# Kernel optimization log

Measured on AMD Instinct MI355X. Metric: run time of the kernel, lower is better.

## Reference

```python
import jax, jax.numpy as jnp
import numpy as np

T, B, H, IN = 2048, 4096, 51, 2

def setup_inputs() -> dict:
    key = jax.random.key(0)
    ks = jax.random.split(key, 12)
    s = 1.0 / np.sqrt(H)
    u = lambda k, shape: jax.random.uniform(k, shape, jnp.float32, -s, s)
    return {
        "input": jax.random.normal(ks[0], (T, B, IN), jnp.float32),
        "W_ih1": u(ks[1], (4 * H, IN)),
        "W_hh1": u(ks[2], (4 * H, H)),
        "b_ih1": u(ks[3], (4 * H,)),
        "b_hh1": u(ks[4], (4 * H,)),
        "W_ih2": u(ks[5], (4 * H, H)),
        "W_hh2": u(ks[6], (4 * H, H)),
        "b_ih2": u(ks[7], (4 * H,)),
        "b_hh2": u(ks[8], (4 * H,)),
        "W_lin": u(ks[9], (1, H)),
        "b_lin": u(ks[10], (1,)),
    }

def _lstm_cell(x, h, c, W_ih, W_hh, b_ih, b_hh):
    # PyTorch LSTMCell gate order: input, forget, cell(g), output
    gates = x @ W_ih.T + b_ih + h @ W_hh.T + b_hh  # [B, 4H]
    i, f, g, o = jnp.split(gates, 4, axis=-1)
    c_new = jax.nn.sigmoid(f) * c + jax.nn.sigmoid(i) * jnp.tanh(g)
    h_new = jax.nn.sigmoid(o) * jnp.tanh(c_new)
    return h_new, c_new

def reference(input, W_ih1, W_hh1, b_ih1, b_hh1, W_ih2, W_hh2, b_ih2, b_hh2, W_lin, b_lin):
    Bsz = input.shape[1]
    z = jnp.zeros((Bsz, H), input.dtype)

    def step(carry, x_t):
        h1, c1, h2, c2 = carry
        h1, c1 = _lstm_cell(x_t, h1, c1, W_ih1, W_hh1, b_ih1, b_hh1)
        h2, c2 = _lstm_cell(h1, h2, c2, W_ih2, W_hh2, b_ih2, b_hh2)
        out = h2 @ W_lin.T + b_lin  # [B, 1]
        return (h1, c1, h2, c2), out[:, 0]

    _, outs = jax.lax.scan(step, (z, z, z, z), input)  # outs: [T, B]
    return outs.T  # [B, T] == torch.stack(outputs, 1).squeeze(2)
```

## Files before the change

kernel.cpp:

```cpp
#include <hip/hip_runtime.h>

namespace {
constexpr int T    = 2048;
constexpr int Bsz  = 4096;
constexpr int H    = 51;
constexpr int H4   = 204;
constexpr int NB   = 16;
constexpr int BLK  = 1024;
constexpr int GRID = Bsz / NB;
constexpr int NITER = T + 4;
constexpr float SCI  = -1.44269504f;
constexpr float SCGP =  2.88539008f;
constexpr float SC2  = -2.88539008f;
}

typedef float    f32x4 __attribute__((ext_vector_type(4)));
typedef _Float16 f16x8 __attribute__((ext_vector_type(8)));
typedef unsigned short u16;

__device__ __forceinline__ float RCP(float x)  { return __builtin_amdgcn_rcpf(x); }
__device__ __forceinline__ float EXP2(float x) { return __builtin_amdgcn_exp2f(x); }

__device__ __forceinline__ float lstm_act(float Gi, float Gf, float Gg, float Go, float& c) {
  float ei = EXP2(Gi), ef = EXP2(Gf), eo = EXP2(Go), eg = EXP2(Gg);
  float pi = 1.f + ei, pf = 1.f + ef, pg = 1.f + eg, po = 1.f + eo;
  float pig = pi * pg;
  float num = fmaf(c, pig, (eg - 1.f) * pf);
  c = num * RCP(pig * pf);
  float ec = EXP2(SC2 * fabsf(c));
  float tc = copysignf(1.f - ec, c);
  return tc * RCP((1.f + ec) * po);
}

#define BAR() asm volatile("s_waitcnt lgkmcnt(0)\n\ts_barrier" ::: "memory")
#define MF(A, B, C) __builtin_amdgcn_mfma_f32_16x16x32_f16((A), (B), (C), 0, 0, 0)


__global__ __launch_bounds__(BLK, 4) void lstm2_v10(
    const float* __restrict__ x,
    const float* __restrict__ Wih1, const float* __restrict__ Whh1,
    const float* __restrict__ bih1, const float* __restrict__ bhh1,
    const float* __restrict__ Wih2, const float* __restrict__ Whh2,
    const float* __restrict__ bih2, const float* __restrict__ bhh2,
    const float* __restrict__ Wlin, const float* __restrict__ blin,
    float* __restrict__ out) {
  extern __shared__ __align__(16) char smraw[];
  u16*   PL1 = (u16*)smraw;
  u16*   PL2 = (u16*)(smraw + 8192);
  auto   XB  = (float2 (*)[32][16])(smraw + 12288);
  auto   OB  = (float (*)[16][40])(smraw + 20480);
  float* SW  = (float*)smraw;

  const int tid  = threadIdx.x;
  const int lane = tid & 63;
  const int wid  = tid >> 6;
  const int a    = lane & 15;
  const int q    = lane >> 4;
  const int b0   = blockIdx.x * NB;
  const int rb   = lane * 8;

  bool isL1 = false; int tA = -1, tB = -1;
  switch (wid) {
    case 0:  isL1 = true; tA = 0;  tB = 1;  break;
    case 1:  isL1 = true; tA = 4;  tB = 5;  break;
    case 2:  isL1 = true; tA = 8;  tB = 9;  break;
    case 3:  isL1 = true; tA = 10; tB = 11; break;
    case 4:  isL1 = true; tA = 2;  tB = 3;  break;
    case 5:  isL1 = true; tA = 6;  tB = 7;  break;
    case 6:  tA = 6;  tB = 7;  break;
    case 7:  isL1 = true; tA = 12; break;
    case 8:  tA = 0;  tB = 1;  break;
    case 9:  tA = 3;  tB = 4;  break;
    case 10: tA = 8;  tB = 9;  break;
    case 11: tA = 10; tB = 11; break;
    case 12: tA = 2;  break;
    case 13: tA = 5;  break;
    case 14: break;
    case 15: tA = 12; break;
  }
  const bool isHead = (wid == 14);
  const bool isXinj = (wid == 15);
  const bool isL2   = (!isL1) && (tA >= 0);

  f16x8 wA[2][4];
  f16x8 hA[2];

  for (int i = tid; i < H4 * H; i += BLK) SW[i] = Whh1[i];
  __syncthreads();
  if (isL1) {
#pragma unroll
    for (int ti = 0; ti < 2; ++ti) {
      const int t = ti ? tB : tA;
      if (t >= 0) {
        const int  rp   = 16 * t + a;
        const bool vld  = (rp < H4);
        const int  gate = rp & 3;
        const int  wrow = gate * H + (rp >> 2);
        const float sc  = (gate == 2) ? SCGP : SCI;
#pragma unroll
        for (int sp = 0; sp < 2; ++sp)
#pragma unroll
          for (int j = 0; j < 8; ++j) {
            const int k = 32 * sp + 16 * (j >> 2) + 4 * q + (j & 3);
            float val = 0.f;
            if (vld) {
              if (k < H)           val = SW[wrow * H + k];
              else if (k == H)     val = Wih1[wrow * 2 + 0];
              else if (k == H + 1) val = Wih1[wrow * 2 + 1];
              else if (k == H + 2) val = bih1[wrow] + bhh1[wrow];
            }
            wA[ti][sp][j] = (_Float16)(val * sc);
          }
      }
    }
  }
  __syncthreads();
  for (int i = tid; i < H4 * H; i += BLK) SW[i] = Wih2[i];
  __syncthreads();
  if (isL2) {
#pragma unroll
    for (int ti = 0; ti < 2; ++ti) {
      const int t = ti ? tB : tA;
      if (t >= 0) {
        const int  rp   = 16 * t + a;
        const bool vld  = (rp < H4);
        const int  gate = rp & 3;
        const int  wrow = gate * H + (rp >> 2);
        const float sc  = (gate == 2) ? SCGP : SCI;
#pragma unroll
        for (int sp = 0; sp < 2; ++sp)
#pragma unroll
          for (int j = 0; j < 8; ++j) {
            const int k = 32 * sp + 16 * (j >> 2) + 4 * q + (j & 3);
            float val = 0.f;
            if (vld) {
              if (k < H)           val = SW[wrow * H + k];
              else if (k == H + 2) val = bih2[wrow] + bhh2[wrow];
            }
            wA[ti][sp][j] = (_Float16)(val * sc);
          }
      }
    }
  }
  __syncthreads();
  for (int i = tid; i < H4 * H; i += BLK) SW[i] = Whh2[i];
  __syncthreads();
  if (isL2) {
#pragma unroll
    for (int ti = 0; ti < 2; ++ti) {
      const int t = ti ? tB : tA;
      if (t >= 0) {
        const int  rp   = 16 * t + a;
        const bool vld  = (rp < H4);
        const int  gate = rp & 3;
        const int  wrow = gate * H + (rp >> 2);
        const float sc  = (gate == 2) ? SCGP : SCI;
#pragma unroll
        for (int sp = 2; sp < 4; ++sp)
#pragma unroll
          for (int j = 0; j < 8; ++j) {
            const int kp = 32 * (sp - 2) + 16 * (j >> 2) + 4 * q + (j & 3);
            float val = (vld && kp < H) ? SW[wrow * H + kp] * sc : 0.f;
            wA[ti][sp][j] = (_Float16)val;
          }
      }
    }
  }
  if (isHead) {
#pragma unroll
    for (int sp = 0; sp < 2; ++sp)
#pragma unroll
      for (int j = 0; j < 8; ++j) {
        const int kp = 32 * sp + 16 * (j >> 2) + 4 * q + (j & 3);
        float val = 0.f;
        if (a == 0) {
          if (kp < H)           val = Wlin[kp];
          else if (kp == H + 2) val = blin[0];
        }
        hA[sp][j] = (_Float16)val;
      }
  }
  __syncthreads();

  for (int i = tid; i < 6144; i += BLK) PL1[i] = 0;
  if (isXinj) {
#pragma unroll
    for (int k = 0; k < 4; ++k) {
      const int idx = lane + 64 * k, st = idx >> 3, bc = (idx & 7) * 2;
      *(float4*)&XB[0][st][bc] = *(const float4*)(x + ((size_t)st * Bsz + b0 + bc) * 2);
    }
  }
  __syncthreads();
  if (tid < 16) {
#pragma unroll
    for (int buf = 0; buf < 4; ++buf) PL1[buf * 1024 + 512 + (tid + 16) * 8 + 5] = 0x3C00;
#pragma unroll
    for (int buf = 0; buf < 2; ++buf) PL2[buf * 1024 + 512 + (tid + 16) * 8 + 5] = 0x3C00;
  }
  __syncthreads();
  const int xslot = ((lane >> 4) == 0) ? (lane & 15) * 8 + 7 : ((lane & 15) + 16) * 8 + 4;
  if (isXinj && lane < 32) {
    const float xv = ((const float*)&XB[0][0][0])[(lane & 15) * 2 + (lane >> 4)];
    *(_Float16*)&PL1[3 * 1024 + 512 + xslot] = (_Float16)xv;
  }
  __syncthreads();

  int  widx0 = 0, widx1 = 0;
  bool uval0 = false, uval1 = false;
  if (tA >= 0) {
    const int u = 4 * tA + q;
    if (u < H) {
      uval0 = true;
      const int spl = u >> 5, kl = u & 31;
      widx0 = spl * 512 + (a + 16 * ((kl >> 2) & 3)) * 8 + ((kl & 3) + 4 * (kl >> 4));
    }
  }
  if (tB >= 0) {
    const int u = 4 * tB + q;
    if (u < H) {
      uval1 = true;
      const int spl = u >> 5, kl = u & 31;
      widx1 = spl * 512 + (a + 16 * ((kl >> 2) & 3)) * 8 + ((kl & 3) + 4 * (kl >> 4));
    }
  }

  float cc0 = 0.f, cc1 = 0.f;
  const f32x4 z4 = {0.f, 0.f, 0.f, 0.f};

  if (isL1) {
    f16x8 pf0 = *(const f16x8*)&PL1[3 * 1024 + rb];
    f16x8 pf1 = *(const f16x8*)&PL1[3 * 1024 + 512 + rb];

#define L1B(S, B)                                                               \
  { const int s = (S);                                                          \
    f32x4 dA = MF(wA[0][0], pf0, z4); dA = MF(wA[0][1], pf1, dA);               \
    f32x4 dB = z4;                                                              \
    if (tB >= 0) { dB = MF(wA[1][0], pf0, z4); dB = MF(wA[1][1], pf1, dB); }    \
    if (s < T) {                                                                \
      const float h0 = lstm_act(dA[0], dA[1], dA[2], dA[3], cc0);               \
      if (uval0) *(_Float16*)&PL1[(B) * 1024 + widx0] = (_Float16)h0;           \
      if (tB >= 0) {                                                            \
        const float h1 = lstm_act(dB[0], dB[1], dB[2], dB[3], cc1);             \
        if (uval1) *(_Float16*)&PL1[(B) * 1024 + widx1] = (_Float16)h1;         \
      }                                                                         \
    }                                                                           \
    BAR();                                                                      \
    pf0 = *(const f16x8*)&PL1[(B) * 1024 + rb];                                 \
    pf1 = *(const f16x8*)&PL1[(B) * 1024 + 512 + rb];                           \
  }

    for (int s0 = 0; s0 < NITER; s0 += 4) {
      L1B(s0 + 0, 0) L1B(s0 + 1, 1) L1B(s0 + 2, 2) L1B(s0 + 3, 3)
    }
#undef L1B
  } else {
    f16x8 pc0 = *(const f16x8*)&PL1[2 * 1024 + rb];
    f16x8 pc1 = *(const f16x8*)&PL1[2 * 1024 + 512 + rb];
    float4 xcr0 = {0,0,0,0}, xcr1 = {0,0,0,0}, xcr2 = {0,0,0,0}, xcr3 = {0,0,0,0};

#define BB(S, B)                                                                \
  { const int s = (S); constexpr int P = (B) & 1;                               \
    f16x8 bq0 = *(const f16x8*)&PL2[(P ^ 1) * 1024 + rb];                       \
    f16x8 bq1 = *(const f16x8*)&PL2[(P ^ 1) * 1024 + 512 + rb];                 \
    if (isXinj) {                                                               \
      const int ph = s & 31;                                                    \
      if (ph == 0) {                                                            \
        if (s + 32 < T) {                                                       \
          const int i0 = lane, i1 = lane + 64, i2 = lane + 128, i3 = lane + 192;\
          xcr0 = *(const float4*)(x + ((size_t)(s + 32 + (i0 >> 3)) * Bsz + b0 + (i0 & 7) * 2) * 2); \
          xcr1 = *(const float4*)(x + ((size_t)(s + 32 + (i1 >> 3)) * Bsz + b0 + (i1 & 7) * 2) * 2); \
          xcr2 = *(const float4*)(x + ((size_t)(s + 32 + (i2 >> 3)) * Bsz + b0 + (i2 & 7) * 2) * 2); \
          xcr3 = *(const float4*)(x + ((size_t)(s + 32 + (i3 >> 3)) * Bsz + b0 + (i3 & 7) * 2) * 2); \
        }                                                                       \
      } else if (ph == 1) {                                                     \
        if (s + 31 < T) {                                                       \
          const int buf = ((s >> 5) + 1) & 1;                                   \
          const int i0 = lane, i1 = lane + 64, i2 = lane + 128, i3 = lane + 192;\
          *(float4*)&XB[buf][i0 >> 3][(i0 & 7) * 2] = xcr0;                     \
          *(float4*)&XB[buf][i1 >> 3][(i1 & 7) * 2] = xcr1;                     \
          *(float4*)&XB[buf][i2 >> 3][(i2 & 7) * 2] = xcr2;                     \
          *(float4*)&XB[buf][i3 >> 3][(i3 & 7) * 2] = xcr3;                     \
        }                                                                       \
      } else if (ph == 3 && s >= 35) {                                          \
        const int f = (s - 35) >> 5;                                            \
        const int r = lane >> 2, c0 = (lane & 3) * 8;                           \
        const float4 v0 = *(const float4*)&OB[f & 1][r][c0];                    \
        const float4 v1 = *(const float4*)&OB[f & 1][r][c0 + 4];                \
        *(float4*)(out + (size_t)(b0 + r) * T + f * 32 + c0)     = v0;          \
        *(float4*)(out + (size_t)(b0 + r) * T + f * 32 + c0 + 4) = v1;          \
      }                                                                         \
    }                                                                           \
    f32x4 dA = z4, dB = z4;                                                     \
    if (tA >= 0) {                                                              \
      dA = MF(wA[0][0], pc0, z4); dA = MF(wA[0][1], pc1, dA);                   \
      if (tB >= 0) { dB = MF(wA[1][0], pc0, z4); dB = MF(wA[1][1], pc1, dB); }  \
      pc0 = *(const f16x8*)&PL1[(((B) + 3) & 3) * 1024 + rb];                   \
      pc1 = *(const f16x8*)&PL1[(((B) + 3) & 3) * 1024 + 512 + rb];             \
      dA = MF(wA[0][2], bq0, dA); dA = MF(wA[0][3], bq1, dA);                   \
      if (tB >= 0) { dB = MF(wA[1][2], bq0, dB); dB = MF(wA[1][3], bq1, dB); }  \
      if (s >= 2 && s <= T + 1) {                                               \
        const float h0 = lstm_act(dA[0], dA[1], dA[2], dA[3], cc0);             \
        if (uval0) *(_Float16*)&PL2[P * 1024 + widx0] = (_Float16)h0;           \
        if (tB >= 0) {                                                          \
          const float h1 = lstm_act(dB[0], dB[1], dB[2], dB[3], cc1);           \
          if (uval1) *(_Float16*)&PL2[P * 1024 + widx1] = (_Float16)h1;         \
        }                                                                       \
      }                                                                         \
    }                                                                           \
    if (isHead) {                                                               \
      f32x4 dh = MF(hA[0], bq0, z4); dh = MF(hA[1], bq1, dh);                   \
      if (s >= 3 && s <= T + 2 && lane < 16)                                    \
        OB[((s - 3) >> 5) & 1][lane][(s - 3) & 31] = dh[0];                     \
    }                                                                           \
    if (isXinj && lane < 32 && s + 1 < T) {                                     \
      const int st = (s + 1) & 31, cb = ((s + 1) >> 5) & 1;                     \
      const float xv = ((const float*)&XB[cb][st][0])[(lane & 15) * 2 + (lane >> 4)]; \
      *(_Float16*)&PL1[(B) * 1024 + 512 + xslot] = (_Float16)xv;                \
    }                                                                           \
    BAR();                                                                      \
  }

    for (int s0 = 0; s0 < NITER; s0 += 4) {
      BB(s0 + 0, 0) BB(s0 + 1, 1) BB(s0 + 2, 2) BB(s0 + 3, 3)
    }
#undef BB
  }
}

extern "C" void kernel_launch(void* const* d_in, const int* in_sizes, int n_in,
                              void* d_out, int out_size, void* d_ws, size_t ws_size,
                              hipStream_t stream) {
  (void)in_sizes; (void)n_in; (void)d_ws; (void)ws_size; (void)out_size;
  const float* x    = (const float*)d_in[0];
  const float* Wih1 = (const float*)d_in[1];
  const float* Whh1 = (const float*)d_in[2];
  const float* bih1 = (const float*)d_in[3];
  const float* bhh1 = (const float*)d_in[4];
  const float* Wih2 = (const float*)d_in[5];
  const float* Whh2 = (const float*)d_in[6];
  const float* bih2 = (const float*)d_in[7];
  const float* bhh2 = (const float*)d_in[8];
  const float* Wlin = (const float*)d_in[9];
  const float* blin = (const float*)d_in[10];
  float* out = (float*)d_out;

  const size_t shmem = (size_t)H4 * H * sizeof(float);
  hipFuncSetAttribute((const void*)lstm2_v10,
                      hipFuncAttributeMaxDynamicSharedMemorySize, (int)shmem);

  hipLaunchKernelGGL(lstm2_v10, dim3(GRID), dim3(BLK), shmem, stream,
                     x, Wih1, Whh1, bih1, bhh1, Wih2, Whh2, bih2, bhh2,
                     Wlin, blin, out);
}
```

Measured before the change: 1.190 ms.

## Rebalance wave roles so waves mix layer-1 and layer-2 tiles

Reassigns the 16 waves so that waves 0-7 each compute one layer-1 tile and one layer-2 tile per step, waves 8-12 do layer-2 tiles only, and waves 13-15 do the remaining layer-1 tiles. Layer-2 now sums two independent MFMA chains (input and recurrent parts) instead of one serial chain of four. The x loading, output writeback and head duties move to different waves, and all shared-memory fragment loads are issued right after the barrier. The aim is to even out per-wave MFMA and activation work between barriers, so the slowest wave in each step does less, at the cost of more registers in the mixed waves.

```diff
diff --git a/kernel.cpp b/kernel.cpp
--- a/kernel.cpp
+++ b/kernel.cpp
@@ -36,7 +36,7 @@
 #define MF(A, B, C) __builtin_amdgcn_mfma_f32_16x16x32_f16((A), (B), (C), 0, 0, 0)
 
 
-__global__ __launch_bounds__(BLK, 4) void lstm2_v10(
+__global__ __launch_bounds__(BLK, 4) void lstm2_v11(
     const float* __restrict__ x,
     const float* __restrict__ Wih1, const float* __restrict__ Whh1,
     const float* __restrict__ bih1, const float* __restrict__ bhh1,
@@ -59,38 +59,28 @@
   const int b0   = blockIdx.x * NB;
   const int rb   = lane * 8;
 
-  bool isL1 = false; int tA = -1, tB = -1;
-  switch (wid) {
-    case 0:  isL1 = true; tA = 0;  tB = 1;  break;
-    case 1:  isL1 = true; tA = 4;  tB = 5;  break;
-    case 2:  isL1 = true; tA = 8;  tB = 9;  break;
-    case 3:  isL1 = true; tA = 10; tB = 11; break;
-    case 4:  isL1 = true; tA = 2;  tB = 3;  break;
-    case 5:  isL1 = true; tA = 6;  tB = 7;  break;
-    case 6:  tA = 6;  tB = 7;  break;
-    case 7:  isL1 = true; tA = 12; break;
-    case 8:  tA = 0;  tB = 1;  break;
-    case 9:  tA = 3;  tB = 4;  break;
-    case 10: tA = 8;  tB = 9;  break;
-    case 11: tA = 10; tB = 11; break;
-    case 12: tA = 2;  break;
-    case 13: tA = 5;  break;
-    case 14: break;
-    case 15: tA = 12; break;
-  }
-  const bool isHead = (wid == 14);
+  int l1A = -1, l1B = -1, l2A = -1;
+  if (wid < 8)        { l1A = wid; l2A = wid; }
+  else if (wid < 13)  { l2A = wid; }
+  else if (wid == 13) { l1A = 8;  l1B = 9;  }
+  else if (wid == 14) { l1A = 10; l1B = 11; }
+  else                { l1A = 12; }
+  const bool isHead = (wid == 12);
+  const bool isXld  = (wid == 8);
   const bool isXinj = (wid == 15);
-  const bool isL2   = (!isL1) && (tA >= 0);
-
-  f16x8 wA[2][4];
+  const bool hasL1  = (l1A >= 0);
+  const bool hasL2  = (l2A >= 0);
+
+  f16x8 wL1[2][2];
+  f16x8 wL2[4];
   f16x8 hA[2];
 
   for (int i = tid; i < H4 * H; i += BLK) SW[i] = Whh1[i];
   __syncthreads();
-  if (isL1) {
+  if (hasL1) {
 #pragma unroll
     for (int ti = 0; ti < 2; ++ti) {
-      const int t = ti ? tB : tA;
+      const int t = ti ? l1B : l1A;
       if (t >= 0) {
         const int  rp   = 16 * t + a;
         const bool vld  = (rp < H4);
@@ -109,7 +99,7 @@
               else if (k == H + 1) val = Wih1[wrow * 2 + 1];
               else if (k == H + 2) val = bih1[wrow] + bhh1[wrow];
             }
-            wA[ti][sp][j] = (_Float16)(val * sc);
+            wL1[ti][sp][j] = (_Float16)(val * sc);
           }
       }
     }
@@ -117,54 +107,42 @@
   __syncthreads();
   for (int i = tid; i < H4 * H; i += BLK) SW[i] = Wih2[i];
   __syncthreads();
-  if (isL2) {
-#pragma unroll
-    for (int ti = 0; ti < 2; ++ti) {
-      const int t = ti ? tB : tA;
-      if (t >= 0) {
-        const int  rp   = 16 * t + a;
-        const bool vld  = (rp < H4);
-        const int  gate = rp & 3;
-        const int  wrow = gate * H + (rp >> 2);
-        const float sc  = (gate == 2) ? SCGP : SCI;
-#pragma unroll
-        for (int sp = 0; sp < 2; ++sp)
-#pragma unroll
-          for (int j = 0; j < 8; ++j) {
-            const int k = 32 * sp + 16 * (j >> 2) + 4 * q + (j & 3);
-            float val = 0.f;
-            if (vld) {
-              if (k < H)           val = SW[wrow * H + k];
-              else if (k == H + 2) val = bih2[wrow] + bhh2[wrow];
-            }
-            wA[ti][sp][j] = (_Float16)(val * sc);
-          }
+  if (hasL2) {
+    const int  rp   = 16 * l2A + a;
+    const bool vld  = (rp < H4);
+    const int  gate = rp & 3;
+    const int  wrow = gate * H + (rp >> 2);
+    const float sc  = (gate == 2) ? SCGP : SCI;
+#pragma unroll
+    for (int sp = 0; sp < 2; ++sp)
+#pragma unroll
+      for (int j = 0; j < 8; ++j) {
+        const int k = 32 * sp + 16 * (j >> 2) + 4 * q + (j & 3);
+        float val = 0.f;
+        if (vld) {
+          if (k < H)           val = SW[wrow * H + k];
+          else if (k == H + 2) val = bih2[wrow] + bhh2[wrow];
+        }
+        wL2[sp][j] = (_Float16)(val * sc);
       }
-    }
   }
   __syncthreads();
   for (int i = tid; i < H4 * H; i += BLK) SW[i] = Whh2[i];
   __syncthreads();
-  if (isL2) {
-#pragma unroll
-    for (int ti = 0; ti < 2; ++ti) {
-      const int t = ti ? tB : tA;
-      if (t >= 0) {
-        const int  rp   = 16 * t + a;
-        const bool vld  = (rp < H4);
-        const int  gate = rp & 3;
-        const int  wrow = gate * H + (rp >> 2);
-        const float sc  = (gate == 2) ? SCGP : SCI;
-#pragma unroll
-        for (int sp = 2; sp < 4; ++sp)
-#pragma unroll
-          for (int j = 0; j < 8; ++j) {
-            const int kp = 32 * (sp - 2) + 16 * (j >> 2) + 4 * q + (j & 3);
-            float val = (vld && kp < H) ? SW[wrow * H + kp] * sc : 0.f;
-            wA[ti][sp][j] = (_Float16)val;
-          }
+  if (hasL2) {
+    const int  rp   = 16 * l2A + a;
+    const bool vld  = (rp < H4);
+    const int  gate = rp & 3;
+    const int  wrow = gate * H + (rp >> 2);
+    const float sc  = (gate == 2) ? SCGP : SCI;
+#pragma unroll
+    for (int sp = 2; sp < 4; ++sp)
+#pragma unroll
+      for (int j = 0; j < 8; ++j) {
+        const int kp = 32 * (sp - 2) + 16 * (j >> 2) + 4 * q + (j & 3);
+        float val = (vld && kp < H) ? SW[wrow * H + kp] * sc : 0.f;
+        wL2[sp][j] = (_Float16)val;
       }
-    }
   }
   if (isHead) {
 #pragma unroll
@@ -183,7 +161,7 @@
   __syncthreads();
 
   for (int i = tid; i < 6144; i += BLK) PL1[i] = 0;
-  if (isXinj) {
+  if (isXld) {
 #pragma unroll
     for (int k = 0; k < 4; ++k) {
       const int idx = lane + 64 * k, st = idx >> 3, bc = (idx & 7) * 2;
@@ -205,64 +183,80 @@
   }
   __syncthreads();
 
-  int  widx0 = 0, widx1 = 0;
-  bool uval0 = false, uval1 = false;
-  if (tA >= 0) {
-    const int u = 4 * tA + q;
+  int  widx1A = 0, widx1B = 0, widx2 = 0;
+  bool uv1A = false, uv1B = false, uv2 = false;
+  if (l1A >= 0) {
+    const int u = 4 * l1A + q;
     if (u < H) {
-      uval0 = true;
+      uv1A = true;
       const int spl = u >> 5, kl = u & 31;
-      widx0 = spl * 512 + (a + 16 * ((kl >> 2) & 3)) * 8 + ((kl & 3) + 4 * (kl >> 4));
-    }
-  }
-  if (tB >= 0) {
-    const int u = 4 * tB + q;
+      widx1A = spl * 512 + (a + 16 * ((kl >> 2) & 3)) * 8 + ((kl & 3) + 4 * (kl >> 4));
+    }
+  }
+  if (l1B >= 0) {
+    const int u = 4 * l1B + q;
     if (u < H) {
-      uval1 = true;
+      uv1B = true;
       const int spl = u >> 5, kl = u & 31;
-      widx1 = spl * 512 + (a + 16 * ((kl >> 2) & 3)) * 8 + ((kl & 3) + 4 * (kl >> 4));
-    }
-  }
-
-  float cc0 = 0.f, cc1 = 0.f;
+      widx1B = spl * 512 + (a + 16 * ((kl >> 2) & 3)) * 8 + ((kl & 3) + 4 * (kl >> 4));
+    }
+  }
+  if (l2A >= 0) {
+    const int u = 4 * l2A + q;
+    if (u < H) {
+      uv2 = true;
+      const int spl = u >> 5, kl = u & 31;
+      widx2 = spl * 512 + (a + 16 * ((kl >> 2) & 3)) * 8 + ((kl & 3) + 4 * (kl >> 4));
+    }
+  }
+
+  float cc1 = 0.f, cc2 = 0.f;
   const f32x4 z4 = {0.f, 0.f, 0.f, 0.f};
 
-  if (isL1) {
+  if (wid < 8) {
     f16x8 pf0 = *(const f16x8*)&PL1[3 * 1024 + rb];
     f16x8 pf1 = *(const f16x8*)&PL1[3 * 1024 + 512 + rb];
-
-#define L1B(S, B)                                                               \
-  { const int s = (S);                                                          \
-    f32x4 dA = MF(wA[0][0], pf0, z4); dA = MF(wA[0][1], pf1, dA);               \
-    f32x4 dB = z4;                                                              \
-    if (tB >= 0) { dB = MF(wA[1][0], pf0, z4); dB = MF(wA[1][1], pf1, dB); }    \
+    f16x8 pc0 = *(const f16x8*)&PL1[2 * 1024 + rb];
+    f16x8 pc1 = *(const f16x8*)&PL1[2 * 1024 + 512 + rb];
+    f16x8 bq0 = *(const f16x8*)&PL2[1 * 1024 + rb];
+    f16x8 bq1 = *(const f16x8*)&PL2[1 * 1024 + 512 + rb];
+
+#define MX(S, B)                                                                \
+  { const int s = (S); const int P = (B) & 1;                                   \
+    f32x4 d1 = MF(wL1[0][0], pf0, z4); d1 = MF(wL1[0][1], pf1, d1);             \
+    f32x4 aP = MF(wL2[0], pc0, z4);    aP = MF(wL2[1], pc1, aP);                \
+    f32x4 aQ = MF(wL2[2], bq0, z4);    aQ = MF(wL2[3], bq1, aQ);                \
     if (s < T) {                                                                \
-      const float h0 = lstm_act(dA[0], dA[1], dA[2], dA[3], cc0);               \
-      if (uval0) *(_Float16*)&PL1[(B) * 1024 + widx0] = (_Float16)h0;           \
-      if (tB >= 0) {                                                            \
-        const float h1 = lstm_act(dB[0], dB[1], dB[2], dB[3], cc1);             \
-        if (uval1) *(_Float16*)&PL1[(B) * 1024 + widx1] = (_Float16)h1;         \
-      }                                                                         \
+      const float h = lstm_act(d1[0], d1[1], d1[2], d1[3], cc1);                \
+      if (uv1A) *(_Float16*)&PL1[(B) * 1024 + widx1A] = (_Float16)h;            \
+    }                                                                           \
+    f32x4 d2 = aP + aQ;                                                         \
+    if (s >= 2 && s <= T + 1) {                                                 \
+      const float h = lstm_act(d2[0], d2[1], d2[2], d2[3], cc2);                \
+      if (uv2) *(_Float16*)&PL2[P * 1024 + widx2] = (_Float16)h;                \
     }                                                                           \
     BAR();                                                                      \
     pf0 = *(const f16x8*)&PL1[(B) * 1024 + rb];                                 \
     pf1 = *(const f16x8*)&PL1[(B) * 1024 + 512 + rb];                           \
-  }
-
+    pc0 = *(const f16x8*)&PL1[(((B) + 3) & 3) * 1024 + rb];                     \
+    pc1 = *(const f16x8*)&PL1[(((B) + 3) & 3) * 1024 + 512 + rb];               \
+    bq0 = *(const f16x8*)&PL2[P * 1024 + rb];                                   \
+    bq1 = *(const f16x8*)&PL2[P * 1024 + 512 + rb];                             \
+  }
     for (int s0 = 0; s0 < NITER; s0 += 4) {
-      L1B(s0 + 0, 0) L1B(s0 + 1, 1) L1B(s0 + 2, 2) L1B(s0 + 3, 3)
-    }
-#undef L1B
-  } else {
+      MX(s0 + 0, 0) MX(s0 + 1, 1) MX(s0 + 2, 2) MX(s0 + 3, 3)
+    }
+#undef MX
+  } else if (hasL2) {
     f16x8 pc0 = *(const f16x8*)&PL1[2 * 1024 + rb];
     f16x8 pc1 = *(const f16x8*)&PL1[2 * 1024 + 512 + rb];
+    f16x8 bq0 = *(const f16x8*)&PL2[1 * 1024 + rb];
+    f16x8 bq1 = *(const f16x8*)&PL2[1 * 1024 + 512 + rb];
     float4 xcr0 = {0,0,0,0}, xcr1 = {0,0,0,0}, xcr2 = {0,0,0,0}, xcr3 = {0,0,0,0};
 
-#define BB(S, B)                                                                \
-  { const int s = (S); constexpr int P = (B) & 1;                               \
-    f16x8 bq0 = *(const f16x8*)&PL2[(P ^ 1) * 1024 + rb];                       \
-    f16x8 bq1 = *(const f16x8*)&PL2[(P ^ 1) * 1024 + 512 + rb];                 \
-    if (isXinj) {                                                               \
+#define L2M(S, B)                                                               \
+  { const int s = (S); const int P = (B) & 1;                                   \
+    if (isXld) {                                                                \
       const int ph = s & 31;                                                    \
       if (ph == 0) {                                                            \
         if (s + 32 < T) {                                                       \
@@ -281,7 +275,20 @@
           *(float4*)&XB[buf][i2 >> 3][(i2 & 7) * 2] = xcr2;                     \
           *(float4*)&XB[buf][i3 >> 3][(i3 & 7) * 2] = xcr3;                     \
         }                                                                       \
-      } else if (ph == 3 && s >= 35) {                                          \
+      }                                                                         \
+    }                                                                           \
+    f32x4 aP = MF(wL2[0], pc0, z4); aP = MF(wL2[1], pc1, aP);                   \
+    f32x4 aQ = MF(wL2[2], bq0, z4); aQ = MF(wL2[3], bq1, aQ);                   \
+    f32x4 d2 = aP + aQ;                                                         \
+    if (s >= 2 && s <= T + 1) {                                                 \
+      const float h = lstm_act(d2[0], d2[1], d2[2], d2[3], cc2);                \
+      if (uv2) *(_Float16*)&PL2[P * 1024 + widx2] = (_Float16)h;                \
+    }                                                                           \
+    if (isHead) {                                                               \
+      f32x4 dh = MF(hA[0], bq0, z4); dh = MF(hA[1], bq1, dh);                   \
+      if (s >= 3 && s <= T + 2 && lane < 16)                                    \
+        OB[((s - 3) >> 5) & 1][lane][(s - 3) & 31] = dh[0];                     \
+      if ((s & 31) == 3 && s >= 35) {                                           \
         const int f = (s - 35) >> 5;                                            \
         const int r = lane >> 2, c0 = (lane & 3) * 8;                           \
         const float4 v0 = *(const float4*)&OB[f & 1][r][c0];                    \
@@ -290,27 +297,32 @@
         *(float4*)(out + (size_t)(b0 + r) * T + f * 32 + c0 + 4) = v1;          \
       }                                                                         \
     }                                                                           \
-    f32x4 dA = z4, dB = z4;                                                     \
-    if (tA >= 0) {                                                              \
-      dA = MF(wA[0][0], pc0, z4); dA = MF(wA[0][1], pc1, dA);                   \
-      if (tB >= 0) { dB = MF(wA[1][0], pc0, z4); dB = MF(wA[1][1], pc1, dB); }  \
-      pc0 = *(const f16x8*)&PL1[(((B) + 3) & 3) * 1024 + rb];                   \
-      pc1 = *(const f16x8*)&PL1[(((B) + 3) & 3) * 1024 + 512 + rb];             \
-      dA = MF(wA[0][2], bq0, dA); dA = MF(wA[0][3], bq1, dA);                   \
-      if (tB >= 0) { dB = MF(wA[1][2], bq0, dB); dB = MF(wA[1][3], bq1, dB); }  \
-      if (s >= 2 && s <= T + 1) {                                               \
-        const float h0 = lstm_act(dA[0], dA[1], dA[2], dA[3], cc0);             \
-        if (uval0) *(_Float16*)&PL2[P * 1024 + widx0] = (_Float16)h0;           \
-        if (tB >= 0) {                                                          \
-          const float h1 = lstm_act(dB[0], dB[1], dB[2], dB[3], cc1);           \
-          if (uval1) *(_Float16*)&PL2[P * 1024 + widx1] = (_Float16)h1;         \
-        }                                                                       \
+    BAR();                                                                      \
+    pc0 = *(const f16x8*)&PL1[(((B) + 3) & 3) * 1024 + rb];                     \
+    pc1 = *(const f16x8*)&PL1[(((B) + 3) & 3) * 1024 + 512 + rb];               \
+    bq0 = *(const f16x8*)&PL2[P * 1024 + rb];                                   \
+    bq1 = *(const f16x8*)&PL2[P * 1024 + 512 + rb];                             \
+  }
+    for (int s0 = 0; s0 < NITER; s0 += 4) {
+      L2M(s0 + 0, 0) L2M(s0 + 1, 1) L2M(s0 + 2, 2) L2M(s0 + 3, 3)
+    }
+#undef L2M
+  } else {
+    f16x8 pf0 = *(const f16x8*)&PL1[3 * 1024 + rb];
+    f16x8 pf1 = *(const f16x8*)&PL1[3 * 1024 + 512 + rb];
+
+#define L1M(S, B)                                                               \
+  { const int s = (S);                                                          \
+    f32x4 dA = MF(wL1[0][0], pf0, z4); dA = MF(wL1[0][1], pf1, dA);             \
+    f32x4 dB = z4;                                                              \
+    if (l1B >= 0) { dB = MF(wL1[1][0], pf0, z4); dB = MF(wL1[1][1], pf1, dB); } \
+    if (s < T) {                                                                \
+      const float h0 = lstm_act(dA[0], dA[1], dA[2], dA[3], cc1);               \
+      if (uv1A) *(_Float16*)&PL1[(B) * 1024 + widx1A] = (_Float16)h0;           \
+      if (l1B >= 0) {                                                           \
+        const float h1 = lstm_act(dB[0], dB[1], dB[2], dB[3], cc2);             \
+        if (uv1B) *(_Float16*)&PL1[(B) * 1024 + widx1B] = (_Float16)h1;         \
       }                                                                         \
-    }                                                                           \
-    if (isHead) {                                                               \
-      f32x4 dh = MF(hA[0], bq0, z4); dh = MF(hA[1], bq1, dh);                   \
-      if (s >= 3 && s <= T + 2 && lane < 16)                                    \
-        OB[((s - 3) >> 5) & 1][lane][(s - 3) & 31] = dh[0];                     \
     }                                                                           \
     if (isXinj && lane < 32 && s + 1 < T) {                                     \
       const int st = (s + 1) & 31, cb = ((s + 1) >> 5) & 1;                     \
@@ -318,12 +330,13 @@
       *(_Float16*)&PL1[(B) * 1024 + 512 + xslot] = (_Float16)xv;                \
     }                                                                           \
     BAR();                                                                      \
-  }
-
+    pf0 = *(const f16x8*)&PL1[(B) * 1024 + rb];                                 \
+    pf1 = *(const f16x8*)&PL1[(B) * 1024 + 512 + rb];                           \
+  }
     for (int s0 = 0; s0 < NITER; s0 += 4) {
-      BB(s0 + 0, 0) BB(s0 + 1, 1) BB(s0 + 2, 2) BB(s0 + 3, 3)
-    }
-#undef BB
+      L1M(s0 + 0, 0) L1M(s0 + 1, 1) L1M(s0 + 2, 2) L1M(s0 + 3, 3)
+    }
+#undef L1M
   }
 }
 
@@ -345,10 +358,10 @@
   float* out = (float*)d_out;
 
   const size_t shmem = (size_t)H4 * H * sizeof(float);
-  hipFuncSetAttribute((const void*)lstm2_v10,
+  hipFuncSetAttribute((const void*)lstm2_v11,
                       hipFuncAttributeMaxDynamicSharedMemorySize, (int)shmem);
 
-  hipLaunchKernelGGL(lstm2_v10, dim3(GRID), dim3(BLK), shmem, stream,
+  hipLaunchKernelGGL(lstm2_v11, dim3(GRID), dim3(BLK), shmem, stream,
                      x, Wih1, Whh1, bih1, bhh1, Wih2, Whh2, bih2, bhh2,
                      Wlin, blin, out);
 }
```

New measurement: 1.196 ms. Within noise of the previous version (+0.5%).

## Split per-step barrier into two phases and reorder layer-2 activation before MFMA

Applied to the files above, without the earlier changes.

Each timestep now uses two block barriers instead of one. Layer 1 separates its MFMA from the activation/write phase, and layer 2 computes its activation from the previous step's accumulators at the start of the step, then syncs and runs the MFMAs for the next step. The buffer indices and step offsets change to match the new pipeline. The aim is to restructure how the layer-1 and layer-2 warps overlap and hand off data, at the cost of an extra barrier per step.

```diff
diff --git a/kernel.cpp b/kernel.cpp
--- a/kernel.cpp
+++ b/kernel.cpp
@@ -36,7 +36,7 @@
 #define MF(A, B, C) __builtin_amdgcn_mfma_f32_16x16x32_f16((A), (B), (C), 0, 0, 0)
 
 
-__global__ __launch_bounds__(BLK, 4) void lstm2_v10(
+__global__ __launch_bounds__(BLK, 4) void lstm2_v13(
     const float* __restrict__ x,
     const float* __restrict__ Wih1, const float* __restrict__ Whh1,
     const float* __restrict__ bih1, const float* __restrict__ bhh1,
@@ -236,6 +236,7 @@
     f32x4 dA = MF(wA[0][0], pf0, z4); dA = MF(wA[0][1], pf1, dA);               \
     f32x4 dB = z4;                                                              \
     if (tB >= 0) { dB = MF(wA[1][0], pf0, z4); dB = MF(wA[1][1], pf1, dB); }    \
+    BAR();                                                             \
     if (s < T) {                                                                \
       const float h0 = lstm_act(dA[0], dA[1], dA[2], dA[3], cc0);               \
       if (uval0) *(_Float16*)&PL1[(B) * 1024 + widx0] = (_Float16)h0;           \
@@ -244,7 +245,7 @@
         if (uval1) *(_Float16*)&PL1[(B) * 1024 + widx1] = (_Float16)h1;         \
       }                                                                         \
     }                                                                           \
-    BAR();                                                                      \
+    BAR();                                                             \
     pf0 = *(const f16x8*)&PL1[(B) * 1024 + rb];                                 \
     pf1 = *(const f16x8*)&PL1[(B) * 1024 + 512 + rb];                           \
   }
@@ -254,14 +255,12 @@
     }
 #undef L1B
   } else {
-    f16x8 pc0 = *(const f16x8*)&PL1[2 * 1024 + rb];
-    f16x8 pc1 = *(const f16x8*)&PL1[2 * 1024 + 512 + rb];
     float4 xcr0 = {0,0,0,0}, xcr1 = {0,0,0,0}, xcr2 = {0,0,0,0}, xcr3 = {0,0,0,0};
+    f32x4 d2A = z4, d2B = z4;
 
 #define BB(S, B)                                                                \
   { const int s = (S); constexpr int P = (B) & 1;                               \
-    f16x8 bq0 = *(const f16x8*)&PL2[(P ^ 1) * 1024 + rb];                       \
-    f16x8 bq1 = *(const f16x8*)&PL2[(P ^ 1) * 1024 + 512 + rb];                 \
+                                                                \
     if (isXinj) {                                                               \
       const int ph = s & 31;                                                    \
       if (ph == 0) {                                                            \
@@ -290,22 +289,29 @@
         *(float4*)(out + (size_t)(b0 + r) * T + f * 32 + c0 + 4) = v1;          \
       }                                                                         \
     }                                                                           \
-    f32x4 dA = z4, dB = z4;                                                     \
+                          \
+    if (tA >= 0 && s >= 3 && s <= T + 2) {                                      \
+      const float h0 = lstm_act(d2A[0], d2A[1], d2A[2], d2A[3], cc0);           \
+      if (uval0) *(_Float16*)&PL2[P * 1024 + widx0] = (_Float16)h0;             \
+      if (tB >= 0) {                                                            \
+        const float h1 = lstm_act(d2B[0], d2B[1], d2B[2], d2B[3], cc1);         \
+        if (uval1) *(_Float16*)&PL2[P * 1024 + widx1] = (_Float16)h1;           \
+      }                                                                         \
+    }                                                                           \
+                                    \
+    f16x8 pc0, pc1;                                                             \
     if (tA >= 0) {                                                              \
-      dA = MF(wA[0][0], pc0, z4); dA = MF(wA[0][1], pc1, dA);                   \
-      if (tB >= 0) { dB = MF(wA[1][0], pc0, z4); dB = MF(wA[1][1], pc1, dB); }  \
-      pc0 = *(const f16x8*)&PL1[(((B) + 3) & 3) * 1024 + rb];                   \
-      pc1 = *(const f16x8*)&PL1[(((B) + 3) & 3) * 1024 + 512 + rb];             \
-      dA = MF(wA[0][2], bq0, dA); dA = MF(wA[0][3], bq1, dA);                   \
-      if (tB >= 0) { dB = MF(wA[1][2], bq0, dB); dB = MF(wA[1][3], bq1, dB); }  \
-      if (s >= 2 && s <= T + 1) {                                               \
-        const float h0 = lstm_act(dA[0], dA[1], dA[2], dA[3], cc0);             \
-        if (uval0) *(_Float16*)&PL2[P * 1024 + widx0] = (_Float16)h0;           \
-        if (tB >= 0) {                                                          \
-          const float h1 = lstm_act(dB[0], dB[1], dB[2], dB[3], cc1);           \
-          if (uval1) *(_Float16*)&PL2[P * 1024 + widx1] = (_Float16)h1;         \
-        }                                                                       \
-      }                                                                         \
+      pc0 = *(const f16x8*)&PL1[(((B) + 2) & 3) * 1024 + rb];                   \
+      pc1 = *(const f16x8*)&PL1[(((B) + 2) & 3) * 1024 + 512 + rb];             \
+    }                                                                           \
+    BAR();                                                             \
+    f16x8 bq0 = *(const f16x8*)&PL2[P * 1024 + rb];                             \
+    f16x8 bq1 = *(const f16x8*)&PL2[P * 1024 + 512 + rb];                       \
+    if (tA >= 0) {                                                              \
+      d2A = MF(wA[0][0], pc0, z4); d2A = MF(wA[0][1], pc1, d2A);                \
+      if (tB >= 0) { d2B = MF(wA[1][0], pc0, z4); d2B = MF(wA[1][1], pc1, d2B); } \
+      d2A = MF(wA[0][2], bq0, d2A); d2A = MF(wA[0][3], bq1, d2A);               \
+      if (tB >= 0) { d2B = MF(wA[1][2], bq0, d2B); d2B = MF(wA[1][3], bq1, d2B); } \
     }                                                                           \
     if (isHead) {                                                               \
       f32x4 dh = MF(hA[0], bq0, z4); dh = MF(hA[1], bq1, dh);                   \
@@ -317,7 +323,7 @@
       const float xv = ((const float*)&XB[cb][st][0])[(lane & 15) * 2 + (lane >> 4)]; \
       *(_Float16*)&PL1[(B) * 1024 + 512 + xslot] = (_Float16)xv;                \
     }                                                                           \
-    BAR();                                                                      \
+    BAR();                                                             \
   }
 
     for (int s0 = 0; s0 < NITER; s0 += 4) {
@@ -345,10 +351,10 @@
   float* out = (float*)d_out;
 
   const size_t shmem = (size_t)H4 * H * sizeof(float);
-  hipFuncSetAttribute((const void*)lstm2_v10,
+  hipFuncSetAttribute((const void*)lstm2_v13,
                       hipFuncAttributeMaxDynamicSharedMemorySize, (int)shmem);
 
-  hipLaunchKernelGGL(lstm2_v10, dim3(GRID), dim3(BLK), shmem, stream,
+  hipLaunchKernelGGL(lstm2_v13, dim3(GRID), dim3(BLK), shmem, stream,
                      x, Wih1, Whh1, bih1, bhh1, Wih2, Whh2, bih2, bhh2,
                      Wlin, blin, out);
 }
```

New measurement: 1.433 ms. 20.4% more time.

## Halve batch columns per block to double grid size and blocks per CU

Applied to the files above, without the earlier changes.

Each block now handles 8 batch columns instead of 16, so the grid doubles to 512 blocks, and launch bounds now ask for 8 resident blocks per CU. The x staging, output buffering and x injection into the MFMA operand are reworked for the narrower tile. The goal is to spread the latency-bound recurrence over more CUs and overlap more blocks. In exchange, half of each 16-wide MFMA column tile sits idle, and the tighter register budget from the higher occupancy target may cause spills.

```diff
diff --git a/kernel.cpp b/kernel.cpp
--- a/kernel.cpp
+++ b/kernel.cpp
@@ -5,7 +5,7 @@
 constexpr int Bsz  = 4096;
 constexpr int H    = 51;
 constexpr int H4   = 204;
-constexpr int NB   = 16;
+constexpr int NB   = 8;
 constexpr int BLK  = 1024;
 constexpr int GRID = Bsz / NB;
 constexpr int NITER = T + 4;
@@ -36,7 +36,7 @@
 #define MF(A, B, C) __builtin_amdgcn_mfma_f32_16x16x32_f16((A), (B), (C), 0, 0, 0)
 
 
-__global__ __launch_bounds__(BLK, 4) void lstm2_v10(
+__global__ __launch_bounds__(BLK, 8) void lstm2_v14(
     const float* __restrict__ x,
     const float* __restrict__ Wih1, const float* __restrict__ Whh1,
     const float* __restrict__ bih1, const float* __restrict__ bhh1,
@@ -47,8 +47,8 @@
   extern __shared__ __align__(16) char smraw[];
   u16*   PL1 = (u16*)smraw;
   u16*   PL2 = (u16*)(smraw + 8192);
-  auto   XB  = (float2 (*)[32][16])(smraw + 12288);
-  auto   OB  = (float (*)[16][40])(smraw + 20480);
+  auto   XB4 = (float4 (*)[32][4])(smraw + 12288);
+  auto   OB  = (float (*)[8][40])(smraw + 16384);
   float* SW  = (float*)smraw;
 
   const int tid  = threadIdx.x;
@@ -185,9 +185,9 @@
   for (int i = tid; i < 6144; i += BLK) PL1[i] = 0;
   if (isXinj) {
 #pragma unroll
-    for (int k = 0; k < 4; ++k) {
-      const int idx = lane + 64 * k, st = idx >> 3, bc = (idx & 7) * 2;
-      *(float4*)&XB[0][st][bc] = *(const float4*)(x + ((size_t)st * Bsz + b0 + bc) * 2);
+    for (int k = 0; k < 2; ++k) {
+      const int idx = lane + 64 * k, st = idx >> 2, v = idx & 3;
+      XB4[0][st][v] = *(const float4*)(x + (size_t)st * Bsz * 2 + b0 * 2 + v * 4);
     }
   }
   __syncthreads();
@@ -198,9 +198,10 @@
     for (int buf = 0; buf < 2; ++buf) PL2[buf * 1024 + 512 + (tid + 16) * 8 + 5] = 0x3C00;
   }
   __syncthreads();
-  const int xslot = ((lane >> 4) == 0) ? (lane & 15) * 8 + 7 : ((lane & 15) + 16) * 8 + 4;
-  if (isXinj && lane < 32) {
-    const float xv = ((const float*)&XB[0][0][0])[(lane & 15) * 2 + (lane >> 4)];
+  const int bb_x = lane & 7, f_x = (lane >> 3) & 1;
+  const int xslot = (f_x == 0) ? bb_x * 8 + 7 : (bb_x + 16) * 8 + 4;
+  if (isXinj && lane < 16) {
+    const float xv = ((const float*)&XB4[0][0][0])[bb_x * 2 + f_x];
     *(_Float16*)&PL1[3 * 1024 + 512 + xslot] = (_Float16)xv;
   }
   __syncthreads();
@@ -256,7 +257,7 @@
   } else {
     f16x8 pc0 = *(const f16x8*)&PL1[2 * 1024 + rb];
     f16x8 pc1 = *(const f16x8*)&PL1[2 * 1024 + 512 + rb];
-    float4 xcr0 = {0,0,0,0}, xcr1 = {0,0,0,0}, xcr2 = {0,0,0,0}, xcr3 = {0,0,0,0};
+    float4 xcr0 = {0,0,0,0}, xcr1 = {0,0,0,0};
 
 #define BB(S, B)                                                                \
   { const int s = (S); constexpr int P = (B) & 1;                               \
@@ -266,28 +267,22 @@
       const int ph = s & 31;                                                    \
       if (ph == 0) {                                                            \
         if (s + 32 < T) {                                                       \
-          const int i0 = lane, i1 = lane + 64, i2 = lane + 128, i3 = lane + 192;\
-          xcr0 = *(const float4*)(x + ((size_t)(s + 32 + (i0 >> 3)) * Bsz + b0 + (i0 & 7) * 2) * 2); \
-          xcr1 = *(const float4*)(x + ((size_t)(s + 32 + (i1 >> 3)) * Bsz + b0 + (i1 & 7) * 2) * 2); \
-          xcr2 = *(const float4*)(x + ((size_t)(s + 32 + (i2 >> 3)) * Bsz + b0 + (i2 & 7) * 2) * 2); \
-          xcr3 = *(const float4*)(x + ((size_t)(s + 32 + (i3 >> 3)) * Bsz + b0 + (i3 & 7) * 2) * 2); \
+          const int i0 = lane, i1 = lane + 64;                                  \
+          xcr0 = *(const float4*)(x + (size_t)(s + 32 + (i0 >> 2)) * Bsz * 2 + b0 * 2 + (i0 & 3) * 4); \
+          xcr1 = *(const float4*)(x + (size_t)(s + 32 + (i1 >> 2)) * Bsz * 2 + b0 * 2 + (i1 & 3) * 4); \
         }                                                                       \
       } else if (ph == 1) {                                                     \
         if (s + 31 < T) {                                                       \
           const int buf = ((s >> 5) + 1) & 1;                                   \
-          const int i0 = lane, i1 = lane + 64, i2 = lane + 128, i3 = lane + 192;\
-          *(float4*)&XB[buf][i0 >> 3][(i0 & 7) * 2] = xcr0;                     \
-          *(float4*)&XB[buf][i1 >> 3][(i1 & 7) * 2] = xcr1;                     \
-          *(float4*)&XB[buf][i2 >> 3][(i2 & 7) * 2] = xcr2;                     \
-          *(float4*)&XB[buf][i3 >> 3][(i3 & 7) * 2] = xcr3;                     \
+          const int i0 = lane, i1 = lane + 64;                                  \
+          XB4[buf][i0 >> 2][i0 & 3] = xcr0;                                     \
+          XB4[buf][i1 >> 2][i1 & 3] = xcr1;                                     \
         }                                                                       \
       } else if (ph == 3 && s >= 35) {                                          \
         const int f = (s - 35) >> 5;                                            \
-        const int r = lane >> 2, c0 = (lane & 3) * 8;                           \
+        const int r = lane >> 3, c0 = (lane & 7) * 4;                           \
         const float4 v0 = *(const float4*)&OB[f & 1][r][c0];                    \
-        const float4 v1 = *(const float4*)&OB[f & 1][r][c0 + 4];                \
-        *(float4*)(out + (size_t)(b0 + r) * T + f * 32 + c0)     = v0;          \
-        *(float4*)(out + (size_t)(b0 + r) * T + f * 32 + c0 + 4) = v1;          \
+        *(float4*)(out + (size_t)(b0 + r) * T + f * 32 + c0) = v0;              \
       }                                                                         \
     }                                                                           \
     f32x4 dA = z4, dB = z4;                                                     \
@@ -309,12 +304,12 @@
     }                                                                           \
     if (isHead) {                                                               \
       f32x4 dh = MF(hA[0], bq0, z4); dh = MF(hA[1], bq1, dh);                   \
-      if (s >= 3 && s <= T + 2 && lane < 16)                                    \
+      if (s >= 3 && s <= T + 2 && lane < 8)                                     \
         OB[((s - 3) >> 5) & 1][lane][(s - 3) & 31] = dh[0];                     \
     }                                                                           \
-    if (isXinj && lane < 32 && s + 1 < T) {                                     \
+    if (isXinj && lane < 16 && s + 1 < T) {                                     \
       const int st = (s + 1) & 31, cb = ((s + 1) >> 5) & 1;                     \
-      const float xv = ((const float*)&XB[cb][st][0])[(lane & 15) * 2 + (lane >> 4)]; \
+      const float xv = ((const float*)&XB4[cb][st][0])[bb_x * 2 + f_x];         \
       *(_Float16*)&PL1[(B) * 1024 + 512 + xslot] = (_Float16)xv;                \
     }                                                                           \
     BAR();                                                                      \
@@ -345,10 +340,10 @@
   float* out = (float*)d_out;
 
   const size_t shmem = (size_t)H4 * H * sizeof(float);
-  hipFuncSetAttribute((const void*)lstm2_v10,
+  hipFuncSetAttribute((const void*)lstm2_v14,
                       hipFuncAttributeMaxDynamicSharedMemorySize, (int)shmem);
 
-  hipLaunchKernelGGL(lstm2_v10, dim3(GRID), dim3(BLK), shmem, stream,
+  hipLaunchKernelGGL(lstm2_v14, dim3(GRID), dim3(BLK), shmem, stream,
                      x, Wih1, Whh1, bih1, bhh1, Wih2, Whh2, bih2, bhh2,
                      Wlin, blin, out);
 }
```

Result: slower. 4.207 ms (+253.6%).
